# Kernel tuning notes

Measured on AMD Instinct MI355X. Metric: run time of the kernel, lower is better.

The kernel has to match this reference:

```python
import jax, jax.numpy as jnp
import numpy as np

N_NODES = 100000


def gcn_conv(x, W, b, src, dst, n):
    # PyG GCNConv: linear transform, add self-loops, symmetric degree norm, scatter-add, bias
    h = x @ W                                      # [n, d_out]
    loop = jnp.arange(n, dtype=src.dtype)
    s = jnp.concatenate([src, loop])               # [E + n]
    d = jnp.concatenate([dst, loop])
    deg = jax.ops.segment_sum(jnp.ones_like(d, dtype=h.dtype), d, num_segments=n)
    dinv = jnp.where(deg > 0, jax.lax.rsqrt(deg), 0.0)
    norm = dinv[s] * dinv[d]                       # [E + n]
    msg = h[s] * norm[:, None]                     # gather + scale
    out = jax.ops.segment_sum(msg, d, num_segments=n)  # scatter-add over targets
    return out + b


def setup_inputs() -> dict:
    key = jax.random.key(0)
    ks = jax.random.split(key, 8)
    n, c_in, hid, c_out = N_NODES, 256, 128, 64
    x = jax.random.normal(ks[0], (n, c_in), dtype=jnp.float32)
    edge_index = jax.random.randint(ks[1], (2, 1600000), 0, n, dtype=jnp.int64)
    s = 0.1
    return {
        "x": x,
        "edge_index": edge_index,
        "W1": jax.random.normal(ks[2], (c_in, hid), dtype=jnp.float32) * s,
        "b1": jnp.zeros((hid,), dtype=jnp.float32),
        "Wmu": jax.random.normal(ks[3], (hid, c_out), dtype=jnp.float32) * s,
        "bmu": jnp.zeros((c_out,), dtype=jnp.float32),
        "Wlv": jax.random.normal(ks[4], (hid, c_out), dtype=jnp.float32) * s,
        "blv": jnp.zeros((c_out,), dtype=jnp.float32),
    }


def reference(x, edge_index, W1, b1, Wmu, bmu, Wlv, blv):
    n = x.shape[0]
    src, dst = edge_index[0], edge_index[1]
    h = jax.nn.relu(gcn_conv(x, W1, b1, src, dst, n))
    mu = gcn_conv(h, Wmu, bmu, src, dst, n)
    logvar = gcn_conv(h, Wlv, blv, src, dst, n)
    return mu, logvar
```

## Files before the change

### kernel.cpp

```cpp
#include <hip/hip_runtime.h>


#define C_IN  256
#define HID   128
#define C_OUT 64
#define NBUCK 1024
#define P1WGS 256

typedef __attribute__((ext_vector_type(8))) short bf16x8;
typedef __attribute__((ext_vector_type(4))) float f32x4;

__device__ inline unsigned short f2bf(float f) {
  unsigned u = __float_as_uint(f);
  unsigned r = u + 0x7FFF + ((u >> 16) & 1);
  return (unsigned short)(r >> 16);
}
__device__ inline float bflo(unsigned v) { return __uint_as_float(v << 16); }
__device__ inline float bfhi(unsigned v) { return __uint_as_float(v & 0xFFFF0000u); }

__global__ __launch_bounds__(256) void k_bin_count(const int* __restrict__ dst,
                                                   int* __restrict__ histmat, int E) {
  __shared__ int h[NBUCK];
  int tid = threadIdx.x;
  for (int i = tid; i < NBUCK; i += 256) h[i] = 0;
  __syncthreads();
  for (int e = blockIdx.x * 256 + tid; e < E; e += P1WGS * 256)
    atomicAdd(&h[dst[e] >> 7], 1);
  __syncthreads();
  for (int i = tid; i < NBUCK; i += 256)
    histmat[blockIdx.x * NBUCK + i] = h[i];
}

__global__ __launch_bounds__(256) void k_col_scan(int* __restrict__ histmat,
                                                  int* __restrict__ bucket_tot) {
  __shared__ int sh[P1WGS];
  int b = blockIdx.x;
  int t = threadIdx.x;
  int v = histmat[t * NBUCK + b];
  sh[t] = v; __syncthreads();
  for (int ofs = 1; ofs < P1WGS; ofs <<= 1) {
    int add = (t >= ofs) ? sh[t - ofs] : 0;
    __syncthreads();
    sh[t] += add;
    __syncthreads();
  }
  histmat[t * NBUCK + b] = sh[t] - v;
  if (t == P1WGS - 1) bucket_tot[b] = sh[t];
}

__global__ void k_bucket_scan(const int* __restrict__ bucket_tot,
                              int* __restrict__ bucket_start, int E) {
  __shared__ int sh[NBUCK];
  int t = threadIdx.x;
  int v = bucket_tot[t];
  sh[t] = v; __syncthreads();
  for (int ofs = 1; ofs < NBUCK; ofs <<= 1) {
    int add = (t >= ofs) ? sh[t - ofs] : 0;
    __syncthreads();
    sh[t] += add;
    __syncthreads();
  }
  bucket_start[t] = sh[t] - v;
  if (t == NBUCK - 1) bucket_start[NBUCK] = E;
}

__global__ __launch_bounds__(256) void k_bin_scatter(const int* __restrict__ src,
                                                     const int* __restrict__ dst,
                                                     const int* __restrict__ histmat,
                                                     const int* __restrict__ bucket_start,
                                                     unsigned* __restrict__ binned, int E) {
  __shared__ int cur[NBUCK];
  int tid = threadIdx.x;
  for (int i = tid; i < NBUCK; i += 256)
    cur[i] = bucket_start[i] + histmat[blockIdx.x * NBUCK + i];
  __syncthreads();
  for (int e = blockIdx.x * 256 + tid; e < E; e += P1WGS * 256) {
    int d = dst[e];
    int pos = atomicAdd(&cur[d >> 7], 1);
    binned[pos] = (unsigned)src[e] | ((unsigned)(d & 127) << 17);
  }
}

__global__ __launch_bounds__(256) void k_bucket_csr(const unsigned* __restrict__ binned,
                                                    const int* __restrict__ bucket_start,
                                                    int* __restrict__ row_start,
                                                    float* __restrict__ dinv,
                                                    int* __restrict__ csr_src,
                                                    int n, int E) {
  __shared__ int h[128], ls[128], c[128];
  int b = blockIdx.x, t = threadIdx.x;
  int start = bucket_start[b], end = bucket_start[b + 1];
  if (t < 128) h[t] = 0;
  __syncthreads();
  for (int e = start + t; e < end; e += 256)
    atomicAdd(&h[binned[e] >> 17], 1);
  __syncthreads();
  if (t < 128) ls[t] = h[t];
  __syncthreads();
  for (int ofs = 1; ofs < 128; ofs <<= 1) {
    int add = (t < 128 && t >= ofs) ? ls[t - ofs] : 0;
    __syncthreads();
    if (t < 128) ls[t] += add;
    __syncthreads();
  }
  if (t < 128) {
    int excl = ls[t] - h[t];
    ls[t] = excl;
    c[t] = excl;
    int node = b * 128 + t;
    if (node < n) {
      row_start[node] = start + excl;
      dinv[node] = rsqrtf((float)h[t] + 1.0f);
    }
  }
  if (b == 0 && t == 0) row_start[n] = E;
  __syncthreads();
  for (int e = start + t; e < end; e += 256) {
    unsigned v = binned[e];
    int pos = start + atomicAdd(&c[v >> 17], 1);
    csr_src[pos] = (int)(v & 0x1FFFF);
  }
}

__global__ void k_prep(const float* __restrict__ W1, const float* __restrict__ Wmu,
                       const float* __restrict__ Wlv,
                       unsigned short* __restrict__ bswz1,
                       unsigned short* __restrict__ bswz2) {
  int idx = blockIdx.x * 256 + threadIdx.x;
  if (idx < 4096) {
    int L = idx & 63, t = (idx >> 6) & 7, s = idx >> 9;
    const float* srcp = W1 + (size_t)(s * 32 + ((L >> 4) << 3)) * 128 + t * 16 + (L & 15);
    unsigned short* dstp = bswz1 + (size_t)idx * 8;
#pragma unroll
    for (int j = 0; j < 8; j++) dstp[j] = f2bf(srcp[(size_t)j * 128]);
  } else if (idx < 6144) {
    int id2 = idx - 4096;
    int L = id2 & 63, t = (id2 >> 6) & 7, s = id2 >> 9;
    int nn = t * 16 + (L & 15);
    int k0 = s * 32 + ((L >> 4) << 3);
    const float* W = (nn < C_OUT) ? (Wmu + nn) : (Wlv + (nn - C_OUT));
    unsigned short* dstp = bswz2 + (size_t)id2 * 8;
#pragma unroll
    for (int j = 0; j < 8; j++) dstp[j] = f2bf(W[(size_t)(k0 + j) * C_OUT]);
  }
}

template <typename AT, int K>
__global__ __launch_bounds__(256) void k_gemm_mfma(const AT* __restrict__ A,
                                                   const unsigned short* __restrict__ bswz,
                                                   unsigned short* __restrict__ C,
                                                   int M) {
  constexpr int NS = K / 32;
  int wave = threadIdx.x >> 6, lane = threadIdx.x & 63;
  int m0 = blockIdx.x * 64 + wave * 16;
  int lrow = lane & 15, lq = lane >> 4;
  int arow = m0 + lrow;
  bool rv = arow < M;
  const AT* ap = A + (size_t)(rv ? arow : 0) * K + lq * 8;

  auto loadA = [&](int s) -> bf16x8 {
    if (sizeof(AT) == 4) {
      const float* af = (const float*)ap + s * 32;
      float4 u0 = rv ? *(const float4*)(af) : float4{0, 0, 0, 0};
      float4 u1 = rv ? *(const float4*)(af + 4) : float4{0, 0, 0, 0};
      union { unsigned short us[8]; bf16x8 v; } tmp;
      tmp.us[0] = f2bf(u0.x); tmp.us[1] = f2bf(u0.y);
      tmp.us[2] = f2bf(u0.z); tmp.us[3] = f2bf(u0.w);
      tmp.us[4] = f2bf(u1.x); tmp.us[5] = f2bf(u1.y);
      tmp.us[6] = f2bf(u1.z); tmp.us[7] = f2bf(u1.w);
      return tmp.v;
    } else {
      const unsigned short* ab = (const unsigned short*)ap + s * 32;
      return rv ? *(const bf16x8*)(ab) : (bf16x8)(short)0;
    }
  };

  f32x4 acc[8];
#pragma unroll
  for (int t = 0; t < 8; t++) acc[t] = (f32x4){0.f, 0.f, 0.f, 0.f};

  bf16x8 a_cur = loadA(0);
  bf16x8 b_cur[8];
#pragma unroll
  for (int t = 0; t < 8; t++)
    b_cur[t] = *(const bf16x8*)(bswz + lane * 8 + t * 512);

#pragma unroll
  for (int s = 0; s < NS; ++s) {
    bf16x8 a_nxt = a_cur;
    bf16x8 b_nxt[8];
    if (s + 1 < NS) {
      a_nxt = loadA(s + 1);
      const unsigned short* bp = bswz + (size_t)(s + 1) * 4096 + lane * 8;
#pragma unroll
      for (int t = 0; t < 8; t++) b_nxt[t] = *(const bf16x8*)(bp + t * 512);
    }
#pragma unroll
    for (int t = 0; t < 8; t++)
      acc[t] = __builtin_amdgcn_mfma_f32_16x16x32_bf16(a_cur, b_cur[t], acc[t], 0, 0, 0);
    a_cur = a_nxt;
    if (s + 1 < NS) {
#pragma unroll
      for (int t = 0; t < 8; t++) b_cur[t] = b_nxt[t];
    }
  }
#pragma unroll
  for (int i = 0; i < 4; i++) {
    int rr = m0 + lq * 4 + i;
    if (rr < M) {
      unsigned short* cp = C + (size_t)rr * 128 + lrow;
#pragma unroll
      for (int t = 0; t < 8; t++) cp[t * 16] = f2bf(acc[t][i]);
    }
  }
}

__device__ inline float rdlane_f(float v, int k) {
  return __uint_as_float(__builtin_amdgcn_readlane(__float_as_uint(v), k));
}

#define AGG_BODY                                                                    \
  int wid = (blockIdx.x * blockDim.x + threadIdx.x) >> 6;                           \
  int lane = threadIdx.x & 63;                                                      \
  if (wid >= n) return;                                                             \
  int rs = row_start[wid], re = row_start[wid + 1];                                 \
  float di = dinv[wid];                                                             \
  float acc0 = 0.f, acc1 = 0.f;                                                     \
  for (int base = rs; base < re + 1; base += 64) {                                  \
    int idx = base + lane;                                                          \
    int sl = wid; float wl = 0.f;                                                   \
    if (idx < re) { sl = csr[idx]; wl = dinv[sl]; }                                 \
    else if (idx == re) { wl = di; }                                 \
    int m = re + 1 - base; if (m > 64) m = 64;                                      \
    int mr = (m + 7) & ~7;                                               \
    for (int k = 0; k < mr; k += 8) {                                               \
      _Pragma("unroll")                                                             \
      for (int j = 0; j < 8; j++) {                                                 \
        int kk = k + j;                                                             \
        int sk = __builtin_amdgcn_readlane(sl, kk);                                 \
        float wk = rdlane_f(wl, kk);                                                \
        unsigned v = *(const unsigned*)(p + (size_t)sk * 128 + 2 * lane);           \
        acc0 += bflo(v) * wk;                                                       \
        acc1 += bfhi(v) * wk;                                                       \
      }                                                                             \
    }                                                                               \
  }                                                                                 \
  acc0 *= di; acc1 *= di;

__global__ __launch_bounds__(256) void k_agg_relu_bf(
    const unsigned short* __restrict__ p, const float* __restrict__ dinv,
    const int* __restrict__ row_start, const int* __restrict__ csr,
    const float* __restrict__ bias, unsigned short* __restrict__ h, int n) {
  AGG_BODY
  float2 bb = *(const float2*)(bias + 2 * lane);
  float r0 = fmaxf(acc0 + bb.x, 0.f);
  float r1 = fmaxf(acc1 + bb.y, 0.f);
  unsigned pk = (unsigned)f2bf(r0) | ((unsigned)f2bf(r1) << 16);
  *(unsigned*)(h + (size_t)wid * 128 + 2 * lane) = pk;
}

__global__ __launch_bounds__(256) void k_agg_out_bf(
    const unsigned short* __restrict__ p, const float* __restrict__ dinv,
    const int* __restrict__ row_start, const int* __restrict__ csr,
    const float* __restrict__ bmu, const float* __restrict__ blv,
    float* __restrict__ out, int n) {
  AGG_BODY
  float2 bb = (lane < 32) ? *(const float2*)(bmu + 2 * lane)
                          : *(const float2*)(blv + 2 * lane - 64);
  float* op = (lane < 32) ? (out + (size_t)wid * C_OUT + 2 * lane)
                          : (out + (size_t)(n + wid) * C_OUT + 2 * lane - 64);
  float2 res = {acc0 + bb.x, acc1 + bb.y};
  *(float2*)op = res;
}

extern "C" void kernel_launch(void* const* d_in, const int* in_sizes, int n_in,
                              void* d_out, int out_size, void* d_ws, size_t ws_size,
                              hipStream_t stream) {
  const float* x   = (const float*)d_in[0];
  const int*   ei  = (const int*)d_in[1];
  const float* W1  = (const float*)d_in[2];
  const float* b1  = (const float*)d_in[3];
  const float* Wmu = (const float*)d_in[4];
  const float* bmu = (const float*)d_in[5];
  const float* Wlv = (const float*)d_in[6];
  const float* blv = (const float*)d_in[7];
  float* out = (float*)d_out;

  const int n = in_sizes[0] / C_IN;
  const int E = in_sizes[1] / 2;
  const int* src = ei;
  const int* dst = ei + E;

  char* w = (char*)d_ws;
  auto alloc = [&](size_t bytes) -> void* {
    void* pp = (void*)w;
    w += (bytes + 255) & ~(size_t)255;
    return pp;
  };
  float*          dinv       = (float*)alloc((size_t)n * 4);
  int*            row_start  = (int*)alloc((size_t)(n + 1) * 4);
  int*            histmat    = (int*)alloc((size_t)P1WGS * NBUCK * 4);
  int*            bucket_tot = (int*)alloc((size_t)NBUCK * 4);
  int*            bucket_st  = (int*)alloc((size_t)(NBUCK + 1) * 4);
  unsigned*       binned     = (unsigned*)alloc((size_t)E * 4);
  int*            csr_src    = (int*)alloc((size_t)E * 4);
  unsigned short* bswz1      = (unsigned short*)alloc((size_t)C_IN * 128 * 2);
  unsigned short* bswz2      = (unsigned short*)alloc((size_t)HID * 128 * 2);
  unsigned short* p1         = (unsigned short*)alloc((size_t)n * 128 * 2);
  unsigned short* hbuf       = (unsigned short*)alloc((size_t)n * 128 * 2);
  unsigned short* p2         = (unsigned short*)alloc((size_t)n * 128 * 2);
  (void)ws_size; (void)n_in; (void)out_size;

  const int TB = 256;
  const int gemm_bks = (n + 63) / 64;
  const int agg_bks = (int)(((size_t)n * 64 + TB - 1) / TB);
  const int nbk_csr = (n + 127) / 128;

  k_bin_count<<<P1WGS, TB, 0, stream>>>(dst, histmat, E);
  k_col_scan<<<NBUCK, TB, 0, stream>>>(histmat, bucket_tot);
  k_bucket_scan<<<1, NBUCK, 0, stream>>>(bucket_tot, bucket_st, E);
  k_bin_scatter<<<P1WGS, TB, 0, stream>>>(src, dst, histmat, bucket_st, binned, E);
  k_bucket_csr<<<nbk_csr, TB, 0, stream>>>(binned, bucket_st, row_start, dinv,
                                           csr_src, n, E);

  k_prep<<<24, 256, 0, stream>>>(W1, Wmu, Wlv, bswz1, bswz2);

  k_gemm_mfma<float, C_IN><<<gemm_bks, TB, 0, stream>>>(x, bswz1, p1, n);
  k_agg_relu_bf<<<agg_bks, TB, 0, stream>>>(p1, dinv, row_start, csr_src, b1, hbuf, n);

  k_gemm_mfma<unsigned short, HID><<<gemm_bks, TB, 0, stream>>>(hbuf, bswz2, p2, n);
  k_agg_out_bf<<<agg_bks, TB, 0, stream>>>(p2, dinv, row_start, csr_src, bmu, blv, out, n);
}
```

Baseline: 406.3 us.

## Pre-scale GEMM rows by dinv and aggregate four nodes per wave with 16B gathers

The source-side degree normalisation is folded into the GEMM epilogue, so each output row is multiplied by dinv before storage. The aggregation then becomes a plain sum with the destination scale applied once. The aggregation kernel now maps four nodes per wave, with 16 lanes each loading 16-byte bf16 vectors. Neighbour indices are broadcast with ds_bpermute, and a zeroed padding row at index n absorbs padded slots. This cuts per-edge dinv gathers and multiplies and widens memory transactions. The cost is warp divergence, since the loop runs to the maximum degree among the four nodes, plus an extra rounding of the pre-scaled values to bf16.

```diff
diff --git a/kernel.cpp b/kernel.cpp
--- a/kernel.cpp
+++ b/kernel.cpp
@@ -125,7 +125,8 @@
 __global__ void k_prep(const float* __restrict__ W1, const float* __restrict__ Wmu,
                        const float* __restrict__ Wlv,
                        unsigned short* __restrict__ bswz1,
-                       unsigned short* __restrict__ bswz2) {
+                       unsigned short* __restrict__ bswz2,
+                       unsigned* __restrict__ p1z, unsigned* __restrict__ p2z) {
   int idx = blockIdx.x * 256 + threadIdx.x;
   if (idx < 4096) {
     int L = idx & 63, t = (idx >> 6) & 7, s = idx >> 9;
@@ -142,6 +143,10 @@
     unsigned short* dstp = bswz2 + (size_t)id2 * 8;
 #pragma unroll
     for (int j = 0; j < 8; j++) dstp[j] = f2bf(W[(size_t)(k0 + j) * C_OUT]);
+  } else if (idx < 6208) {
+    p1z[idx - 6144] = 0u;
+  } else if (idx < 6272) {
+    p2z[idx - 6208] = 0u;
   }
 }
 
@@ -149,6 +154,7 @@
 __global__ __launch_bounds__(256) void k_gemm_mfma(const AT* __restrict__ A,
                                                    const unsigned short* __restrict__ bswz,
                                                    unsigned short* __restrict__ C,
+                                                   const float* __restrict__ dinv,
                                                    int M) {
   constexpr int NS = K / 32;
   int wave = threadIdx.x >> 6, lane = threadIdx.x & 63;
@@ -208,55 +214,90 @@
   for (int i = 0; i < 4; i++) {
     int rr = m0 + lq * 4 + i;
     if (rr < M) {
+      float dsc = dinv[rr];
       unsigned short* cp = C + (size_t)rr * 128 + lrow;
 #pragma unroll
-      for (int t = 0; t < 8; t++) cp[t * 16] = f2bf(acc[t][i]);
-    }
-  }
-}
-
-__device__ inline float rdlane_f(float v, int k) {
-  return __uint_as_float(__builtin_amdgcn_readlane(__float_as_uint(v), k));
-}
-
-#define AGG_BODY                                                                    \
-  int wid = (blockIdx.x * blockDim.x + threadIdx.x) >> 6;                           \
-  int lane = threadIdx.x & 63;                                                      \
-  if (wid >= n) return;                                                             \
-  int rs = row_start[wid], re = row_start[wid + 1];                                 \
-  float di = dinv[wid];                                                             \
-  float acc0 = 0.f, acc1 = 0.f;                                                     \
-  for (int base = rs; base < re + 1; base += 64) {                                  \
-    int idx = base + lane;                                                          \
-    int sl = wid; float wl = 0.f;                                                   \
-    if (idx < re) { sl = csr[idx]; wl = dinv[sl]; }                                 \
-    else if (idx == re) { wl = di; }                                 \
-    int m = re + 1 - base; if (m > 64) m = 64;                                      \
-    int mr = (m + 7) & ~7;                                               \
-    for (int k = 0; k < mr; k += 8) {                                               \
-      _Pragma("unroll")                                                             \
-      for (int j = 0; j < 8; j++) {                                                 \
-        int kk = k + j;                                                             \
-        int sk = __builtin_amdgcn_readlane(sl, kk);                                 \
-        float wk = rdlane_f(wl, kk);                                                \
-        unsigned v = *(const unsigned*)(p + (size_t)sk * 128 + 2 * lane);           \
-        acc0 += bflo(v) * wk;                                                       \
-        acc1 += bfhi(v) * wk;                                                       \
-      }                                                                             \
+      for (int t = 0; t < 8; t++) cp[t * 16] = f2bf(acc[t][i] * dsc);
+    }
+  }
+}
+
+#define AGG_V4_BODY                                                                 \
+  int tid = threadIdx.x;                                                            \
+  int wid4 = blockIdx.x * 4 + (tid >> 6);                  \
+  int lane = tid & 63;                                                              \
+  int li = lane & 15;                                                               \
+  int node = (wid4 << 2) + (lane >> 4);                                             \
+  int rs = 0, re = -1;                                                              \
+  if (node < n) { rs = row_start[node]; re = row_start[node + 1]; }                 \
+  int mc = re - rs + 1;                                       \
+  mc = max(mc, __shfl_xor(mc, 16, 64));                                             \
+  mc = max(mc, __shfl_xor(mc, 32, 64));                                             \
+  int maxcnt = __builtin_amdgcn_readfirstlane(mc);                                  \
+  const char* pb = (const char*)p;                                                  \
+  unsigned loff = (unsigned)(li << 4);                                              \
+  int vb = (lane & 48) << 2;          \
+  float acc[8];                                                                     \
+  _Pragma("unroll")                                                                 \
+  for (int j = 0; j < 8; ++j) acc[j] = 0.f;                                         \
+  for (int t0 = 0; t0 < maxcnt; t0 += 16) {                                         \
+    int s = rs + t0 + li;                                                           \
+    int sl = n;                                                       \
+    if (s < re) sl = csr[s];                                                        \
+    else if (s == re) sl = node;                                     \
+    int km = maxcnt - t0; if (km > 16) km = 16;                                     \
+    for (int k = 0; k < km; k += 4) {                                               \
+      int sk0 = __builtin_amdgcn_ds_bpermute(vb + ((k + 0) << 2), sl);              \
+      int sk1 = __builtin_amdgcn_ds_bpermute(vb + ((k + 1) << 2), sl);              \
+      int sk2 = __builtin_amdgcn_ds_bpermute(vb + ((k + 2) << 2), sl);              \
+      int sk3 = __builtin_amdgcn_ds_bpermute(vb + ((k + 3) << 2), sl);              \
+      uint4 v0 = *(const uint4*)(pb + ((((unsigned)sk0) << 8) + loff));             \
+      uint4 v1 = *(const uint4*)(pb + ((((unsigned)sk1) << 8) + loff));             \
+      uint4 v2 = *(const uint4*)(pb + ((((unsigned)sk2) << 8) + loff));             \
+      uint4 v3 = *(const uint4*)(pb + ((((unsigned)sk3) << 8) + loff));             \
+      acc[0] += bflo(v0.x); acc[1] += bfhi(v0.x);                                   \
+      acc[2] += bflo(v0.y); acc[3] += bfhi(v0.y);                                   \
+      acc[4] += bflo(v0.z); acc[5] += bfhi(v0.z);                                   \
+      acc[6] += bflo(v0.w); acc[7] += bfhi(v0.w);                                   \
+      acc[0] += bflo(v1.x); acc[1] += bfhi(v1.x);                                   \
+      acc[2] += bflo(v1.y); acc[3] += bfhi(v1.y);                                   \
+      acc[4] += bflo(v1.z); acc[5] += bfhi(v1.z);                                   \
+      acc[6] += bflo(v1.w); acc[7] += bfhi(v1.w);                                   \
+      acc[0] += bflo(v2.x); acc[1] += bfhi(v2.x);                                   \
+      acc[2] += bflo(v2.y); acc[3] += bfhi(v2.y);                                   \
+      acc[4] += bflo(v2.z); acc[5] += bfhi(v2.z);                                   \
+      acc[6] += bflo(v2.w); acc[7] += bfhi(v2.w);                                   \
+      acc[0] += bflo(v3.x); acc[1] += bfhi(v3.x);                                   \
+      acc[2] += bflo(v3.y); acc[3] += bfhi(v3.y);                                   \
+      acc[4] += bflo(v3.z); acc[5] += bfhi(v3.z);                                   \
+      acc[6] += bflo(v3.w); acc[7] += bfhi(v3.w);                                   \
     }                                                                               \
-  }                                                                                 \
-  acc0 *= di; acc1 *= di;
+  }
 
 __global__ __launch_bounds__(256) void k_agg_relu_bf(
     const unsigned short* __restrict__ p, const float* __restrict__ dinv,
     const int* __restrict__ row_start, const int* __restrict__ csr,
     const float* __restrict__ bias, unsigned short* __restrict__ h, int n) {
-  AGG_BODY
-  float2 bb = *(const float2*)(bias + 2 * lane);
-  float r0 = fmaxf(acc0 + bb.x, 0.f);
-  float r1 = fmaxf(acc1 + bb.y, 0.f);
-  unsigned pk = (unsigned)f2bf(r0) | ((unsigned)f2bf(r1) << 16);
-  *(unsigned*)(h + (size_t)wid * 128 + 2 * lane) = pk;
+  AGG_V4_BODY
+  if (node < n) {
+    float di = dinv[node];
+    float4 ba = *(const float4*)(bias + (li << 3));
+    float4 bb = *(const float4*)(bias + (li << 3) + 4);
+    float r0 = fmaxf(acc[0] * di + ba.x, 0.f);
+    float r1 = fmaxf(acc[1] * di + ba.y, 0.f);
+    float r2 = fmaxf(acc[2] * di + ba.z, 0.f);
+    float r3 = fmaxf(acc[3] * di + ba.w, 0.f);
+    float r4 = fmaxf(acc[4] * di + bb.x, 0.f);
+    float r5 = fmaxf(acc[5] * di + bb.y, 0.f);
+    float r6 = fmaxf(acc[6] * di + bb.z, 0.f);
+    float r7 = fmaxf(acc[7] * di + bb.w, 0.f);
+    uint4 u;
+    u.x = (unsigned)f2bf(r0) | ((unsigned)f2bf(r1) << 16);
+    u.y = (unsigned)f2bf(r2) | ((unsigned)f2bf(r3) << 16);
+    u.z = (unsigned)f2bf(r4) | ((unsigned)f2bf(r5) << 16);
+    u.w = (unsigned)f2bf(r6) | ((unsigned)f2bf(r7) << 16);
+    *(uint4*)((char*)h + (((size_t)node) << 8) + loff) = u;
+  }
 }
 
 __global__ __launch_bounds__(256) void k_agg_out_bf(
@@ -264,13 +305,21 @@
     const int* __restrict__ row_start, const int* __restrict__ csr,
     const float* __restrict__ bmu, const float* __restrict__ blv,
     float* __restrict__ out, int n) {
-  AGG_BODY
-  float2 bb = (lane < 32) ? *(const float2*)(bmu + 2 * lane)
-                          : *(const float2*)(blv + 2 * lane - 64);
-  float* op = (lane < 32) ? (out + (size_t)wid * C_OUT + 2 * lane)
-                          : (out + (size_t)(n + wid) * C_OUT + 2 * lane - 64);
-  float2 res = {acc0 + bb.x, acc1 + bb.y};
-  *(float2*)op = res;
+  AGG_V4_BODY
+  if (node < n) {
+    float di = dinv[node];
+    const float* bp = (li < 8) ? (bmu + (li << 3)) : (blv + ((li - 8) << 3));
+    float* op = (li < 8) ? (out + (size_t)node * C_OUT + (li << 3))
+                         : (out + (size_t)(n + node) * C_OUT + ((li - 8) << 3));
+    float4 b0 = *(const float4*)(bp);
+    float4 b1 = *(const float4*)(bp + 4);
+    float4 o0 = {acc[0] * di + b0.x, acc[1] * di + b0.y,
+                 acc[2] * di + b0.z, acc[3] * di + b0.w};
+    float4 o1 = {acc[4] * di + b1.x, acc[5] * di + b1.y,
+                 acc[6] * di + b1.z, acc[7] * di + b1.w};
+    *(float4*)op = o0;
+    *(float4*)(op + 4) = o1;
+  }
 }
 
 extern "C" void kernel_launch(void* const* d_in, const int* in_sizes, int n_in,
@@ -306,14 +355,14 @@
   int*            csr_src    = (int*)alloc((size_t)E * 4);
   unsigned short* bswz1      = (unsigned short*)alloc((size_t)C_IN * 128 * 2);
   unsigned short* bswz2      = (unsigned short*)alloc((size_t)HID * 128 * 2);
-  unsigned short* p1         = (unsigned short*)alloc((size_t)n * 128 * 2);
+  unsigned short* p1         = (unsigned short*)alloc((size_t)(n + 1) * 128 * 2);
   unsigned short* hbuf       = (unsigned short*)alloc((size_t)n * 128 * 2);
-  unsigned short* p2         = (unsigned short*)alloc((size_t)n * 128 * 2);
+  unsigned short* p2         = (unsigned short*)alloc((size_t)(n + 1) * 128 * 2);
   (void)ws_size; (void)n_in; (void)out_size;
 
   const int TB = 256;
   const int gemm_bks = (n + 63) / 64;
-  const int agg_bks = (int)(((size_t)n * 64 + TB - 1) / TB);
+  const int agg_bks = (n + 15) / 16;
   const int nbk_csr = (n + 127) / 128;
 
   k_bin_count<<<P1WGS, TB, 0, stream>>>(dst, histmat, E);
@@ -323,11 +372,13 @@
   k_bucket_csr<<<nbk_csr, TB, 0, stream>>>(binned, bucket_st, row_start, dinv,
                                            csr_src, n, E);
 
-  k_prep<<<24, 256, 0, stream>>>(W1, Wmu, Wlv, bswz1, bswz2);
-
-  k_gemm_mfma<float, C_IN><<<gemm_bks, TB, 0, stream>>>(x, bswz1, p1, n);
+  k_prep<<<25, 256, 0, stream>>>(W1, Wmu, Wlv, bswz1, bswz2,
+                                 (unsigned*)(p1 + (size_t)n * 128),
+                                 (unsigned*)(p2 + (size_t)n * 128));
+
+  k_gemm_mfma<float, C_IN><<<gemm_bks, TB, 0, stream>>>(x, bswz1, p1, dinv, n);
   k_agg_relu_bf<<<agg_bks, TB, 0, stream>>>(p1, dinv, row_start, csr_src, b1, hbuf, n);
 
-  k_gemm_mfma<unsigned short, HID><<<gemm_bks, TB, 0, stream>>>(hbuf, bswz2, p2, n);
+  k_gemm_mfma<unsigned short, HID><<<gemm_bks, TB, 0, stream>>>(hbuf, bswz2, p2, dinv, n);
   k_agg_out_bf<<<agg_bks, TB, 0, stream>>>(p2, dinv, row_start, csr_src, bmu, blv, out, n);
 }
```

New measurement: 404.3 us. About the same (-0.5%).
